# Kernel tuning notes

Measured on AMD Instinct MI355X. Metric: run time of the kernel, lower is better.

The kernel has to match this reference:

```python
import jax, jax.numpy as jnp
import numpy as np
import math

B, T, D = 2, 2048, 1024
H, HS = 16, 64  # n_heads, head_size; D == H*HS


def setup_inputs() -> dict:
    key = jax.random.key(0)
    k1, k2, k3 = jax.random.split(key, 3)
    x = jax.random.normal(k1, (B, T, D), dtype=jnp.float32)
    w_qkv = jax.random.normal(k2, (D, 3 * D), dtype=jnp.float32) * (1.0 / math.sqrt(D))
    b_qkv = jnp.zeros((3 * D,), dtype=jnp.float32)
    w_out = jax.random.normal(k3, (D, D), dtype=jnp.float32) * (1.0 / math.sqrt(D))
    b_out = jnp.zeros((D,), dtype=jnp.float32)
    return {"x": x, "w_qkv": w_qkv, "b_qkv": b_qkv, "w_out": w_out, "b_out": b_out}


def reference(x, w_qkv, b_qkv, w_out, b_out):
    b, t, d = x.shape
    qkv = x @ w_qkv + b_qkv                       # (B,T,3D)
    q, k, v = jnp.split(qkv, 3, axis=-1)
    # (B,T,D) -> (B,H,T,HS)
    q = q.reshape(b, t, H, HS).transpose(0, 2, 1, 3)
    k = k.reshape(b, t, H, HS).transpose(0, 2, 1, 3)
    v = v.reshape(b, t, H, HS).transpose(0, 2, 1, 3)
    scale = 1.0 / math.sqrt(HS)
    attn = jnp.einsum('bhqd,bhkd->bhqk', q, k) * scale  # (B,H,T,T)
    causal = jnp.tril(jnp.ones((t, t), dtype=bool))
    attn = jnp.where(causal[None, None], attn, -jnp.inf)
    attn = jax.nn.softmax(attn, axis=-1)
    o = jnp.einsum('bhqk,bhkd->bhqd', attn, v)          # (B,H,T,HS)
    o = o.transpose(0, 2, 1, 3).reshape(b, t, d)
    return o @ w_out + b_out
```

## Files before the change

### kernel.cpp

```cpp
#include <hip/hip_runtime.h>
#include <math.h>

#define B_  2
#define T_  2048
#define D_  1024
#define H_  16
#define HS_ 64
#define M_  (B_*T_)

typedef __bf16 bf16x8 __attribute__((ext_vector_type(8)));
typedef float  f32x4  __attribute__((ext_vector_type(4)));
typedef unsigned short u16;

static __device__ __forceinline__ u16 f2bf(float f) {
    unsigned int u = __float_as_uint(f);
    u += 0x7fff + ((u >> 16) & 1);
    return (u16)(u >> 16);
}

static __device__ __forceinline__ void glds16(const u16* g, u16* l) {
    __builtin_amdgcn_global_load_lds(
        (const __attribute__((address_space(1))) void*)g,
        (__attribute__((address_space(3))) void*)l, 16, 0, 0);
}

__global__ void cast_kernel(const float* __restrict__ in, u16* __restrict__ out) {
    int i = (blockIdx.x * blockDim.x + threadIdx.x) * 4;
    float4 v = *reinterpret_cast<const float4*>(in + i);
    ushort4 o;
    o.x = f2bf(v.x); o.y = f2bf(v.y); o.z = f2bf(v.z); o.w = f2bf(v.w);
    *reinterpret_cast<ushort4*>(out + i) = o;
}

__global__ void transpose_cast(const float* __restrict__ in, u16* __restrict__ out,
                               int R, int C) {
    __shared__ float tile[32][33];
    int c0 = blockIdx.x * 32, r0 = blockIdx.y * 32;
    int tx = threadIdx.x, ty = threadIdx.y;
    #pragma unroll
    for (int j = 0; j < 4; ++j)
        tile[ty + j*8][tx] = in[(size_t)(r0 + ty + j*8) * C + c0 + tx];
    __syncthreads();
    #pragma unroll
    for (int j = 0; j < 4; ++j)
        out[(size_t)(c0 + ty + j*8) * R + r0 + tx] = f2bf(tile[tx][ty + j*8]);
}

template<int MODE>
__global__ __launch_bounds__(256) void gemm_bt(
    const u16* __restrict__ A, const u16* __restrict__ Bt,
    const float* __restrict__ bias,
    float* __restrict__ Cf,
    u16* __restrict__ Qb, u16* __restrict__ Kb, u16* __restrict__ Vt,
    int M, int N, int K)
{
    __shared__ u16 As[128][32];
    __shared__ u16 Bs[128][32];
    int tid  = threadIdx.x;
    int lane = tid & 63, wave = tid >> 6;
    int wm = wave >> 1, wn = wave & 1;
    int quad = lane >> 4, lr = lane & 15;
    int bm = blockIdx.x, bn = blockIdx.y;

    f32x4 acc[4][4] = {};

    const u16* Ab = A  + (size_t)(bm * 128) * K;
    const u16* Bb = Bt + (size_t)(bn * 128) * K;

    int r0 = tid >> 2,           c0 = (tid & 3) * 8;
    int r1 = (tid + 256) >> 2,   c1 = ((tid + 256) & 3) * 8;

    for (int k0 = 0; k0 < K; k0 += 32) {
        __syncthreads();
        glds16(Ab + (size_t)r0 * K + k0 + c0, &As[r0][c0]);
        glds16(Ab + (size_t)r1 * K + k0 + c1, &As[r1][c1]);
        glds16(Bb + (size_t)r0 * K + k0 + c0, &Bs[r0][c0]);
        glds16(Bb + (size_t)r1 * K + k0 + c1, &Bs[r1][c1]);
        __syncthreads();
        bf16x8 af[4], bfr[4];
        #pragma unroll
        for (int i = 0; i < 4; ++i)
            af[i] = *reinterpret_cast<const bf16x8*>(&As[wm*64 + i*16 + lr][quad*8]);
        #pragma unroll
        for (int j = 0; j < 4; ++j)
            bfr[j] = *reinterpret_cast<const bf16x8*>(&Bs[wn*64 + j*16 + lr][quad*8]);
        #pragma unroll
        for (int i = 0; i < 4; ++i)
            #pragma unroll
            for (int j = 0; j < 4; ++j)
                acc[i][j] = __builtin_amdgcn_mfma_f32_16x16x32_bf16(af[i], bfr[j], acc[i][j], 0, 0, 0);
    }

    #pragma unroll
    for (int i = 0; i < 4; ++i) {
        int mrow = bm*128 + wm*64 + i*16 + quad*4;
        #pragma unroll
        for (int j = 0; j < 4; ++j) {
            int ncol = bn*128 + wn*64 + j*16 + lr;
            float bv = bias[ncol];
            #pragma unroll
            for (int r = 0; r < 4; ++r) {
                float v = acc[i][j][r] + bv;
                int m = mrow + r;
                if (MODE == 1) {
                    Cf[(size_t)m * N + ncol] = v;
                } else {
                    int b = m >> 11, t = m & (T_ - 1);
                    int s = ncol >> 10, rem = ncol & 1023;
                    int h = rem >> 6, d = rem & 63;
                    int bh = b * H_ + h;
                    if (s == 0)      Qb[((size_t)bh*T_ + t)*HS_ + d] = f2bf(v * 0.125f);
                    else if (s == 1) Kb[((size_t)bh*T_ + t)*HS_ + d] = f2bf(v);
                    else             Vt[((size_t)bh*HS_ + d)*T_ + t] = f2bf(v);
                }
            }
        }
    }
}

__global__ __launch_bounds__(512) void attn_kernel(
    const u16* __restrict__ Qb, const u16* __restrict__ Kb,
    const u16* __restrict__ Vt, u16* __restrict__ Ob)
{
    __shared__ u16 Ks[64][72];
    __shared__ u16 Vs[64][72];
    __shared__ u16 Ps[8][16][72];

    int tid  = threadIdx.x;
    int lane = tid & 63, wave = tid >> 6;
    int quad = lane >> 4, lr = lane & 15;

    int lin = blockIdx.x;
    int bh  = (lin & 7) + 8 * ((lin >> 3) & 3);
    int p   = lin >> 5;

    int grp   = wave >> 2;
    int myqt  = grp ? (31 - p) : p;
    int jdiag = myqt;
    int jmax  = 31 - p;
    int qw    = myqt * 64 + (wave & 3) * 16;

    const u16* Qp = Qb + ((size_t)bh * T_ + qw) * HS_;
    bf16x8 qf[2];
    #pragma unroll
    for (int h2 = 0; h2 < 2; ++h2)
        qf[h2] = *reinterpret_cast<const bf16x8*>(Qp + lr*HS_ + h2*32 + quad*8);

    f32x4 Oa[4] = {};
    float lrow[4] = {0.f, 0.f, 0.f, 0.f};

    int srow = tid >> 3, scol = (tid & 7) * 8;
    const u16* Kst = Kb + ((size_t)bh*T_ + srow)*HS_ + scol;
    const u16* Vst = Vt + ((size_t)bh*HS_ + srow)*T_ + scol;

    bf16x8 kpre = *reinterpret_cast<const bf16x8*>(Kst);
    bf16x8 vpre = *reinterpret_cast<const bf16x8*>(Vst);

    for (int jt = 0; jt <= jmax; ++jt) {
        __syncthreads();
        *reinterpret_cast<bf16x8*>(&Ks[srow][scol]) = kpre;
        *reinterpret_cast<bf16x8*>(&Vs[srow][scol]) = vpre;
        if (jt < jmax) {
            int kn = (jt + 1) * 64;
            kpre = *reinterpret_cast<const bf16x8*>(Kst + (size_t)kn * HS_);
            vpre = *reinterpret_cast<const bf16x8*>(Vst + kn);
        }
        __syncthreads();

        if (jt <= jdiag) {
            int kb = jt * 64;
            f32x4 Sa[4];
            #pragma unroll
            for (int nt = 0; nt < 4; ++nt) {
                f32x4 z = {};
                bf16x8 b0 = *reinterpret_cast<const bf16x8*>(&Ks[nt*16 + lr][quad*8]);
                bf16x8 b1 = *reinterpret_cast<const bf16x8*>(&Ks[nt*16 + lr][32 + quad*8]);
                z = __builtin_amdgcn_mfma_f32_16x16x32_bf16(qf[0], b0, z, 0, 0, 0);
                z = __builtin_amdgcn_mfma_f32_16x16x32_bf16(qf[1], b1, z, 0, 0, 0);
                Sa[nt] = z;
            }

            if (jt == jdiag) {
                #pragma unroll
                for (int nt = 0; nt < 4; ++nt)
                    #pragma unroll
                    for (int r = 0; r < 4; ++r) {
                        int kg = kb + nt*16 + lr;
                        int qg = qw + quad*4 + r;
                        if (kg > qg) Sa[nt][r] = -INFINITY;
                    }
            }

            #pragma unroll
            for (int nt = 0; nt < 4; ++nt)
                #pragma unroll
                for (int r = 0; r < 4; ++r) {
                    float pv = __expf(Sa[nt][r]);
                    lrow[r] += pv;
                    Ps[wave][quad*4 + r][nt*16 + lr] = f2bf(pv);
                }

            #pragma unroll
            for (int kk = 0; kk < 2; ++kk) {
                bf16x8 pa = *reinterpret_cast<const bf16x8*>(&Ps[wave][lr][kk*32 + quad*8]);
                #pragma unroll
                for (int nt = 0; nt < 4; ++nt) {
                    bf16x8 vb = *reinterpret_cast<const bf16x8*>(&Vs[nt*16 + lr][kk*32 + quad*8]);
                    Oa[nt] = __builtin_amdgcn_mfma_f32_16x16x32_bf16(pa, vb, Oa[nt], 0, 0, 0);
                }
            }
        }
    }

    int b = bh >> 4, h = bh & 15;
    #pragma unroll
    for (int r = 0; r < 4; ++r) {
        float s = lrow[r];
        #pragma unroll
        for (int off = 8; off >= 1; off >>= 1)
            s += __shfl_xor(s, off, 64);
        float inv = 1.f / s;
        int qg = qw + quad*4 + r;
        #pragma unroll
        for (int nt = 0; nt < 4; ++nt) {
            int d = nt*16 + lr;
            Ob[((size_t)b*T_ + qg)*D_ + h*HS_ + d] = f2bf(Oa[nt][r] * inv);
        }
    }
}

extern "C" void kernel_launch(void* const* d_in, const int* in_sizes, int n_in,
                              void* d_out, int out_size, void* d_ws, size_t ws_size,
                              hipStream_t stream) {
    (void)in_sizes; (void)n_in; (void)out_size; (void)ws_size;
    const float* x     = (const float*)d_in[0];
    const float* w_qkv = (const float*)d_in[1];
    const float* b_qkv = (const float*)d_in[2];
    const float* w_out = (const float*)d_in[3];
    const float* b_out = (const float*)d_in[4];
    float* out = (float*)d_out;

    char* ws = (char*)d_ws;
    u16* Xb    = (u16*)ws; ws += (size_t)M_ * D_ * 2;
    u16* WqkvT = (u16*)ws; ws += (size_t)3 * D_ * D_ * 2;
    u16* WoutT = (u16*)ws; ws += (size_t)D_ * D_ * 2;
    u16* Qb    = (u16*)ws; ws += (size_t)M_ * D_ * 2;
    u16* Kb    = (u16*)ws; ws += (size_t)M_ * D_ * 2;
    u16* Vt    = (u16*)ws; ws += (size_t)M_ * D_ * 2;
    u16* Ob    = (u16*)ws; ws += (size_t)M_ * D_ * 2;

    cast_kernel<<<M_ * D_ / 1024, 256, 0, stream>>>(x, Xb);
    transpose_cast<<<dim3(3*D_/32, D_/32), dim3(32, 8), 0, stream>>>(w_qkv, WqkvT, D_, 3*D_);
    transpose_cast<<<dim3(D_/32,   D_/32), dim3(32, 8), 0, stream>>>(w_out, WoutT, D_, D_);
    gemm_bt<0><<<dim3(M_/128, 3*D_/128), 256, 0, stream>>>(
        Xb, WqkvT, b_qkv, nullptr, Qb, Kb, Vt, M_, 3*D_, D_);
    attn_kernel<<<512, 512, 0, stream>>>(Qb, Kb, Vt, Ob);
    gemm_bt<1><<<dim3(M_/128, D_/128), 256, 0, stream>>>(
        Ob, WoutT, b_out, out, nullptr, nullptr, nullptr, M_, D_, D_);
}
```

Before: 191.9 us.

## Use XOR-swizzled LDS, BK=64 GEMM tiles, and 32-row attention waves

The GEMM K-step grows from 32 to 64, and the LDS tiles use an XOR-swizzled 16-byte chunk layout in place of padding, to cut bank conflicts and halve the number of barriers. The attention kernel drops to 256 threads, with each wave handling 32 query rows (two 16-row MFMA tiles). This lets each K/V fragment read from LDS be reused across two MMAs, and the same swizzle is applied to the K, V and P buffers. In exchange, each wave holds more registers and there are fewer waves per block, which may lower occupancy.

```diff
diff --git a/kernel.cpp b/kernel.cpp
--- a/kernel.cpp
+++ b/kernel.cpp
@@ -22,6 +22,10 @@
     __builtin_amdgcn_global_load_lds(
         (const __attribute__((address_space(1))) void*)g,
         (__attribute__((address_space(3))) void*)l, 16, 0, 0);
+}
+
+static __device__ __forceinline__ bf16x8 lds_chunk(const u16* base, int row, int c) {
+    return *reinterpret_cast<const bf16x8*>(base + (size_t)(row * 8 + (c ^ (row & 7))) * 8);
 }
 
 __global__ void cast_kernel(const float* __restrict__ in, u16* __restrict__ out) {
@@ -54,8 +58,8 @@
     u16* __restrict__ Qb, u16* __restrict__ Kb, u16* __restrict__ Vt,
     int M, int N, int K)
 {
-    __shared__ u16 As[128][32];
-    __shared__ u16 Bs[128][32];
+    __shared__ u16 As[128 * 64];
+    __shared__ u16 Bs[128 * 64];
     int tid  = threadIdx.x;
     int lane = tid & 63, wave = tid >> 6;
     int wm = wave >> 1, wn = wave & 1;
@@ -67,28 +71,34 @@
     const u16* Ab = A  + (size_t)(bm * 128) * K;
     const u16* Bb = Bt + (size_t)(bn * 128) * K;
 
-    int r0 = tid >> 2,           c0 = (tid & 3) * 8;
-    int r1 = (tid + 256) >> 2,   c1 = ((tid + 256) & 3) * 8;
-
-    for (int k0 = 0; k0 < K; k0 += 32) {
+    int srow = tid >> 3;
+    int scol = ((tid & 7) ^ (srow & 7)) * 8;
+
+    for (int k0 = 0; k0 < K; k0 += 64) {
         __syncthreads();
-        glds16(Ab + (size_t)r0 * K + k0 + c0, &As[r0][c0]);
-        glds16(Ab + (size_t)r1 * K + k0 + c1, &As[r1][c1]);
-        glds16(Bb + (size_t)r0 * K + k0 + c0, &Bs[r0][c0]);
-        glds16(Bb + (size_t)r1 * K + k0 + c1, &Bs[r1][c1]);
+        #pragma unroll
+        for (int t = 0; t < 4; ++t)
+            glds16(Ab + (size_t)(srow + 32*t) * K + k0 + scol, As + (size_t)(tid + 256*t) * 8);
+        #pragma unroll
+        for (int t = 0; t < 4; ++t)
+            glds16(Bb + (size_t)(srow + 32*t) * K + k0 + scol, Bs + (size_t)(tid + 256*t) * 8);
         __syncthreads();
-        bf16x8 af[4], bfr[4];
-        #pragma unroll
-        for (int i = 0; i < 4; ++i)
-            af[i] = *reinterpret_cast<const bf16x8*>(&As[wm*64 + i*16 + lr][quad*8]);
-        #pragma unroll
-        for (int j = 0; j < 4; ++j)
-            bfr[j] = *reinterpret_cast<const bf16x8*>(&Bs[wn*64 + j*16 + lr][quad*8]);
-        #pragma unroll
-        for (int i = 0; i < 4; ++i)
+        #pragma unroll
+        for (int kk = 0; kk < 2; ++kk) {
+            bf16x8 af[4], bfr[4];
+            int c = kk * 4 + quad;
+            #pragma unroll
+            for (int i = 0; i < 4; ++i)
+                af[i] = lds_chunk(As, wm*64 + i*16 + lr, c);
             #pragma unroll
             for (int j = 0; j < 4; ++j)
-                acc[i][j] = __builtin_amdgcn_mfma_f32_16x16x32_bf16(af[i], bfr[j], acc[i][j], 0, 0, 0);
+                bfr[j] = lds_chunk(Bs, wn*64 + j*16 + lr, c);
+            #pragma unroll
+            for (int i = 0; i < 4; ++i)
+                #pragma unroll
+                for (int j = 0; j < 4; ++j)
+                    acc[i][j] = __builtin_amdgcn_mfma_f32_16x16x32_bf16(af[i], bfr[j], acc[i][j], 0, 0, 0);
+        }
     }
 
     #pragma unroll
@@ -118,13 +128,13 @@
     }
 }
 
-__global__ __launch_bounds__(512) void attn_kernel(
+__global__ __launch_bounds__(256) void attn_kernel(
     const u16* __restrict__ Qb, const u16* __restrict__ Kb,
     const u16* __restrict__ Vt, u16* __restrict__ Ob)
 {
-    __shared__ u16 Ks[64][72];
-    __shared__ u16 Vs[64][72];
-    __shared__ u16 Ps[8][16][72];
+    __shared__ u16 Ks[64 * 64];
+    __shared__ u16 Vs[64 * 64];
+    __shared__ u16 Ps[4][32 * 64];
 
     int tid  = threadIdx.x;
     int lane = tid & 63, wave = tid >> 6;
@@ -134,99 +144,129 @@
     int bh  = (lin & 7) + 8 * ((lin >> 3) & 3);
     int p   = lin >> 5;
 
-    int grp   = wave >> 2;
-    int myqt  = grp ? (31 - p) : p;
-    int jdiag = myqt;
-    int jmax  = 31 - p;
-    int qw    = myqt * 64 + (wave & 3) * 16;
-
-    const u16* Qp = Qb + ((size_t)bh * T_ + qw) * HS_;
-    bf16x8 qf[2];
-    #pragma unroll
-    for (int h2 = 0; h2 < 2; ++h2)
-        qf[h2] = *reinterpret_cast<const bf16x8*>(Qp + lr*HS_ + h2*32 + quad*8);
-
-    f32x4 Oa[4] = {};
-    float lrow[4] = {0.f, 0.f, 0.f, 0.f};
-
-    int srow = tid >> 3, scol = (tid & 7) * 8;
-    const u16* Kst = Kb + ((size_t)bh*T_ + srow)*HS_ + scol;
-    const u16* Vst = Vt + ((size_t)bh*HS_ + srow)*T_ + scol;
-
-    bf16x8 kpre = *reinterpret_cast<const bf16x8*>(Kst);
-    bf16x8 vpre = *reinterpret_cast<const bf16x8*>(Vst);
+    int grp  = wave >> 1;
+    int wg   = wave & 1;
+    int myst = grp ? (31 - p) : p;
+    int qb   = myst * 64 + wg * 32;
+    int jd   = myst;
+    int jmax = 31 - p;
+
+    bf16x8 qf[2][2];
+    #pragma unroll
+    for (int mi = 0; mi < 2; ++mi)
+        #pragma unroll
+        for (int h2 = 0; h2 < 2; ++h2)
+            qf[mi][h2] = *reinterpret_cast<const bf16x8*>(
+                Qb + ((size_t)bh*T_ + qb + mi*16 + lr)*HS_ + h2*32 + quad*8);
+
+    f32x4 Oa[2][4] = {};
+    float lrow[2][4] = {};
+
+    int srow = tid >> 3;
+    int scol = ((tid & 7) ^ (srow & 7)) * 8;
+    const u16* Kst0 = Kb + ((size_t)bh*T_ + srow     )*HS_ + scol;
+    const u16* Kst1 = Kb + ((size_t)bh*T_ + srow + 32)*HS_ + scol;
+    const u16* Vst0 = Vt + ((size_t)bh*HS_ + srow     )*T_ + scol;
+    const u16* Vst1 = Vt + ((size_t)bh*HS_ + srow + 32)*T_ + scol;
+
+    bf16x8 kpre0 = *reinterpret_cast<const bf16x8*>(Kst0);
+    bf16x8 kpre1 = *reinterpret_cast<const bf16x8*>(Kst1);
+    bf16x8 vpre0 = *reinterpret_cast<const bf16x8*>(Vst0);
+    bf16x8 vpre1 = *reinterpret_cast<const bf16x8*>(Vst1);
 
     for (int jt = 0; jt <= jmax; ++jt) {
         __syncthreads();
-        *reinterpret_cast<bf16x8*>(&Ks[srow][scol]) = kpre;
-        *reinterpret_cast<bf16x8*>(&Vs[srow][scol]) = vpre;
+        reinterpret_cast<bf16x8*>(Ks)[tid]       = kpre0;
+        reinterpret_cast<bf16x8*>(Ks)[tid + 256] = kpre1;
+        reinterpret_cast<bf16x8*>(Vs)[tid]       = vpre0;
+        reinterpret_cast<bf16x8*>(Vs)[tid + 256] = vpre1;
         if (jt < jmax) {
-            int kn = (jt + 1) * 64;
-            kpre = *reinterpret_cast<const bf16x8*>(Kst + (size_t)kn * HS_);
-            vpre = *reinterpret_cast<const bf16x8*>(Vst + kn);
+            size_t kn = (size_t)(jt + 1) * 64;
+            kpre0 = *reinterpret_cast<const bf16x8*>(Kst0 + kn * HS_);
+            kpre1 = *reinterpret_cast<const bf16x8*>(Kst1 + kn * HS_);
+            vpre0 = *reinterpret_cast<const bf16x8*>(Vst0 + kn);
+            vpre1 = *reinterpret_cast<const bf16x8*>(Vst1 + kn);
         }
         __syncthreads();
 
-        if (jt <= jdiag) {
+        if (jt <= jd) {
             int kb = jt * 64;
-            f32x4 Sa[4];
-            #pragma unroll
-            for (int nt = 0; nt < 4; ++nt) {
-                f32x4 z = {};
-                bf16x8 b0 = *reinterpret_cast<const bf16x8*>(&Ks[nt*16 + lr][quad*8]);
-                bf16x8 b1 = *reinterpret_cast<const bf16x8*>(&Ks[nt*16 + lr][32 + quad*8]);
-                z = __builtin_amdgcn_mfma_f32_16x16x32_bf16(qf[0], b0, z, 0, 0, 0);
-                z = __builtin_amdgcn_mfma_f32_16x16x32_bf16(qf[1], b1, z, 0, 0, 0);
-                Sa[nt] = z;
-            }
-
-            if (jt == jdiag) {
+            f32x4 Sa[2][4] = {};
+            #pragma unroll
+            for (int kk = 0; kk < 2; ++kk) {
+                int c = kk * 4 + quad;
+                #pragma unroll
+                for (int nt = 0; nt < 4; ++nt) {
+                    bf16x8 bk = lds_chunk(Ks, nt*16 + lr, c);
+                    #pragma unroll
+                    for (int mi = 0; mi < 2; ++mi)
+                        Sa[mi][nt] = __builtin_amdgcn_mfma_f32_16x16x32_bf16(
+                            qf[mi][kk], bk, Sa[mi][nt], 0, 0, 0);
+                }
+            }
+
+            if (jt == jd) {
+                #pragma unroll
+                for (int mi = 0; mi < 2; ++mi)
+                    #pragma unroll
+                    for (int nt = 0; nt < 4; ++nt)
+                        #pragma unroll
+                        for (int r = 0; r < 4; ++r) {
+                            int kg = kb + nt*16 + lr;
+                            int qg = qb + mi*16 + quad*4 + r;
+                            if (kg > qg) Sa[mi][nt][r] = -INFINITY;
+                        }
+            }
+
+            #pragma unroll
+            for (int mi = 0; mi < 2; ++mi)
                 #pragma unroll
                 for (int nt = 0; nt < 4; ++nt)
                     #pragma unroll
                     for (int r = 0; r < 4; ++r) {
-                        int kg = kb + nt*16 + lr;
-                        int qg = qw + quad*4 + r;
-                        if (kg > qg) Sa[nt][r] = -INFINITY;
+                        float pv = __expf(Sa[mi][nt][r]);
+                        lrow[mi][r] += pv;
+                        int prow = mi*16 + quad*4 + r;
+                        int c = nt*2 + (lr >> 3);
+                        Ps[wave][(size_t)(prow*8 + (c ^ (prow & 7)))*8 + (lr & 7)] = f2bf(pv);
                     }
-            }
-
-            #pragma unroll
-            for (int nt = 0; nt < 4; ++nt)
-                #pragma unroll
-                for (int r = 0; r < 4; ++r) {
-                    float pv = __expf(Sa[nt][r]);
-                    lrow[r] += pv;
-                    Ps[wave][quad*4 + r][nt*16 + lr] = f2bf(pv);
+
+            #pragma unroll
+            for (int kk = 0; kk < 2; ++kk) {
+                int c = kk * 4 + quad;
+                bf16x8 pa[2];
+                #pragma unroll
+                for (int mi = 0; mi < 2; ++mi)
+                    pa[mi] = lds_chunk(Ps[wave], mi*16 + lr, c);
+                #pragma unroll
+                for (int nt = 0; nt < 4; ++nt) {
+                    bf16x8 vb = lds_chunk(Vs, nt*16 + lr, c);
+                    #pragma unroll
+                    for (int mi = 0; mi < 2; ++mi)
+                        Oa[mi][nt] = __builtin_amdgcn_mfma_f32_16x16x32_bf16(
+                            pa[mi], vb, Oa[mi][nt], 0, 0, 0);
                 }
-
-            #pragma unroll
-            for (int kk = 0; kk < 2; ++kk) {
-                bf16x8 pa = *reinterpret_cast<const bf16x8*>(&Ps[wave][lr][kk*32 + quad*8]);
-                #pragma unroll
-                for (int nt = 0; nt < 4; ++nt) {
-                    bf16x8 vb = *reinterpret_cast<const bf16x8*>(&Vs[nt*16 + lr][kk*32 + quad*8]);
-                    Oa[nt] = __builtin_amdgcn_mfma_f32_16x16x32_bf16(pa, vb, Oa[nt], 0, 0, 0);
-                }
             }
         }
     }
 
     int b = bh >> 4, h = bh & 15;
     #pragma unroll
-    for (int r = 0; r < 4; ++r) {
-        float s = lrow[r];
-        #pragma unroll
-        for (int off = 8; off >= 1; off >>= 1)
-            s += __shfl_xor(s, off, 64);
-        float inv = 1.f / s;
-        int qg = qw + quad*4 + r;
-        #pragma unroll
-        for (int nt = 0; nt < 4; ++nt) {
-            int d = nt*16 + lr;
-            Ob[((size_t)b*T_ + qg)*D_ + h*HS_ + d] = f2bf(Oa[nt][r] * inv);
-        }
-    }
+    for (int mi = 0; mi < 2; ++mi)
+        #pragma unroll
+        for (int r = 0; r < 4; ++r) {
+            float s = lrow[mi][r];
+            #pragma unroll
+            for (int off = 8; off >= 1; off >>= 1)
+                s += __shfl_xor(s, off, 64);
+            float inv = 1.f / s;
+            int qg = qb + mi*16 + quad*4 + r;
+            #pragma unroll
+            for (int nt = 0; nt < 4; ++nt) {
+                int d = nt*16 + lr;
+                Ob[((size_t)b*T_ + qg)*D_ + h*HS_ + d] = f2bf(Oa[mi][nt][r] * inv);
+            }
+        }
 }
 
 extern "C" void kernel_launch(void* const* d_in, const int* in_sizes, int n_in,
@@ -254,7 +294,7 @@
     transpose_cast<<<dim3(D_/32,   D_/32), dim3(32, 8), 0, stream>>>(w_out, WoutT, D_, D_);
     gemm_bt<0><<<dim3(M_/128, 3*D_/128), 256, 0, stream>>>(
         Xb, WqkvT, b_qkv, nullptr, Qb, Kb, Vt, M_, 3*D_, D_);
-    attn_kernel<<<512, 512, 0, stream>>>(Qb, Kb, Vt, Ob);
+    attn_kernel<<<512, 256, 0, stream>>>(Qb, Kb, Vt, Ob);
     gemm_bt<1><<<dim3(M_/128, D_/128), 256, 0, stream>>>(
         Ob, WoutT, b_out, out, nullptr, nullptr, nullptr, M_, D_, D_);
 }
```

Measured after the change: 210.0 us. 9.4% more time.
